# Performance work log

Measured on AMD Instinct MI355X. Metric: run time of the kernel, lower is better.

## Reference

```python
import jax, jax.numpy as jnp
import numpy as np

N = 50000
E = 800000
IN_DIM = 128
HID = 64
HEADS = 4
OUT_DIM = 128


def setup_inputs() -> dict:
    key = jax.random.key(0)
    ks = jax.random.split(key, 12)
    s = lambda fan: 1.0 / np.sqrt(fan)
    return {
        'features': jax.random.normal(ks[0], (N, IN_DIM), jnp.float32),
        'edge_index': jax.random.randint(ks[1], (2, E), 0, N, jnp.int64),
        # layer 1: in_dim -> heads*hid, concat=True
        'W1': jax.random.normal(ks[2], (IN_DIM, HEADS * HID), jnp.float32) * s(IN_DIM),
        'att_src1': jax.random.normal(ks[3], (HEADS, HID), jnp.float32) * s(HID),
        'att_dst1': jax.random.normal(ks[4], (HEADS, HID), jnp.float32) * s(HID),
        'bias1': jnp.zeros((HEADS * HID,), jnp.float32),
        # layer 2: heads*hid -> out_dim, 1 head, concat=False
        'W2': jax.random.normal(ks[5], (HEADS * HID, OUT_DIM), jnp.float32) * s(HEADS * HID),
        'att_src2': jax.random.normal(ks[6], (1, OUT_DIM), jnp.float32) * s(OUT_DIM),
        'att_dst2': jax.random.normal(ks[7], (1, OUT_DIM), jnp.float32) * s(OUT_DIM),
        'bias2': jnp.zeros((OUT_DIM,), jnp.float32),
    }


def _gat_conv(x, src, dst, W, a_src, a_dst, bias, heads, out_ch):
    n = x.shape[0]
    h = (x @ W).reshape(n, heads, out_ch)              # [N, H, C]
    alpha_s = jnp.einsum('nhc,hc->nh', h, a_src)       # [N, H]
    alpha_d = jnp.einsum('nhc,hc->nh', h, a_dst)
    e = jax.nn.leaky_relu(alpha_s[src] + alpha_d[dst], 0.2)  # [E, H]
    # segment softmax over incoming edges of each dst node
    m = jax.ops.segment_max(e, dst, num_segments=n)
    m = jnp.where(jnp.isfinite(m), m, 0.0)
    ex = jnp.exp(e - m[dst])
    denom = jax.ops.segment_sum(ex, dst, num_segments=n)
    alpha = ex / denom[dst]                            # [E, H]
    out = jax.ops.segment_sum(alpha[:, :, None] * h[src], dst, num_segments=n)  # [N, H, C]
    return out.reshape(n, heads * out_ch) + bias


def reference(features, edge_index, W1, att_src1, att_dst1, bias1, W2, att_src2, att_dst2, bias2):
    n = features.shape[0]
    loops = jnp.arange(n, dtype=edge_index.dtype)
    src = jnp.concatenate([edge_index[0], loops])
    dst = jnp.concatenate([edge_index[1], loops])

    act = lambda v: jax.nn.leaky_relu(v, 0.2)
    x = _gat_conv(features, src, dst, W1, att_src1, att_dst1, bias1, HEADS, HID)
    x = act(x)  # dropout inactive (eval)
    x = _gat_conv(x, src, dst, W2, att_src2, att_dst2, bias2, 1, OUT_DIM)
    x = act(x)
    # in_dim == out_dim -> identity residual
    return x + features
```

## Files before the change

kernel.cpp:

```cpp
#include <hip/hip_runtime.h>
#include <math.h>

#define LRELU(x) ((x) > 0.0f ? (x) : 0.2f * (x))

typedef __attribute__((ext_vector_type(8))) short bf16x8;
typedef __attribute__((ext_vector_type(4))) float floatx4;
typedef __attribute__((ext_vector_type(2))) float f32x2;

__device__ __forceinline__ float bf2f(ushort u) {
    union { unsigned u; float f; } v; v.u = ((unsigned)u) << 16; return v.f;
}
__device__ __forceinline__ ushort f2bf(float f) {
    union { float f; unsigned u; } v; v.f = f;
    unsigned r = (v.u + 0x7FFFu + ((v.u >> 16) & 1u)) >> 16;
    return (ushort)r;
}
__device__ __forceinline__ f32x2 bfpair(unsigned w) {
    union { unsigned u; float f; } lo, hi;
    lo.u = w << 16; hi.u = w & 0xffff0000u;
    return (f32x2){lo.f, hi.f};
}

__global__ __launch_bounds__(256) void prep_kernel(
    const float* __restrict__ feat, const float* __restrict__ W1,
    const float* __restrict__ as1, const float* __restrict__ ad1,
    const float* __restrict__ W2, const float* __restrict__ as2,
    const float* __restrict__ ad2, const int* __restrict__ ei,
    ushort* __restrict__ featb, ushort* __restrict__ Bp1, ushort* __restrict__ Bp2,
    int* __restrict__ deg, ushort* __restrict__ col,
    int N, int E, int Npart, int b_fil, int b_cvt, int b_p1)
{
    const int b = blockIdx.x, t = threadIdx.x;
    if (b < b_fil) {
        const int fb = b;
        const int part = fb & 7;
        const int base = (fb >> 3) * 2048;
        const int lo = part * Npart;
        const int hi = min(N, lo + Npart);
        for (int q0 = 0; q0 < 8; q0 += 4) {
            int dsts[4]; bool val[4];
#pragma unroll
            for (int u = 0; u < 4; ++u) {
                int k = base + (q0 + u) * 256 + t;
                val[u] = k < E;
                if (val[u]) dsts[u] = ei[E + k];
            }
#pragma unroll
            for (int u = 0; u < 4; ++u) {
                if (val[u] && dsts[u] >= lo && dsts[u] < hi) {
                    int k = base + (q0 + u) * 256 + t;
                    int src = ei[k];
                    int slot = atomicAdd(&deg[dsts[u]], 1);
                    if (slot < 63) col[dsts[u] * 64 + slot] = (ushort)src;
                }
            }
        }
    } else if (b < b_fil + b_cvt) {
        int i = (b - b_fil) * 256 + t;
        if (i < N * 32) {
            float4 v = ((const float4*)feat)[i];
            ushort4 o;
            o.x = f2bf(v.x); o.y = f2bf(v.y); o.z = f2bf(v.z); o.w = f2bf(v.w);
            ((ushort4*)featb)[i] = o;
        }
    } else if (b < b_fil + b_cvt + b_p1) {
        int i = (b - b_fil - b_cvt) * 256 + t;
        if (i < 272 * 128) {
            int n = i / 128, k = i % 128;
            float v;
            if (n < 256) v = W1[k * 256 + n];
            else if (n < 260) {
                int h = n - 256; float s = 0.f;
                for (int c = 0; c < 64; ++c) s += W1[k * 256 + h * 64 + c] * as1[h * 64 + c];
                v = s;
            } else if (n < 264) {
                int h = n - 260; float s = 0.f;
                for (int c = 0; c < 64; ++c) s += W1[k * 256 + h * 64 + c] * ad1[h * 64 + c];
                v = s;
            } else v = 0.f;
            Bp1[i] = f2bf(v);
        }
    } else {
        int i = (b - b_fil - b_cvt - b_p1) * 256 + t;
        if (i < 144 * 256) {
            int n = i / 256, k = i % 256;
            float v;
            if (n < 128) v = W2[k * 128 + n];
            else if (n == 128) {
                float s = 0.f;
                for (int c = 0; c < 128; ++c) s += W2[k * 128 + c] * as2[c];
                v = s;
            } else if (n == 129) {
                float s = 0.f;
                for (int c = 0; c < 128; ++c) s += W2[k * 128 + c] * ad2[c];
                v = s;
            } else v = 0.f;
            Bp2[i] = f2bf(v);
        }
    }
}

__global__ __launch_bounds__(256) void gemm_attn1_kernel(
    const ushort* __restrict__ A, const ushort* __restrict__ Bp,
    float* __restrict__ as_, float* __restrict__ ad_, int M)
{
    const int lane = threadIdx.x & 63;
    const int wave = threadIdx.x >> 6;
    const int quad = lane >> 4;
    const int l16  = lane & 15;
    const int row0 = blockIdx.x * 64 + wave * 16;
    const int arow = min(row0 + l16, M - 1);
    const ushort* ap = A + (size_t)arow * 128 + quad * 8;
    const ushort* bp = Bp + (size_t)(256 + l16) * 128 + quad * 8;

    floatx4 acc = (floatx4){0.f, 0.f, 0.f, 0.f};
#pragma unroll
    for (int k0 = 0; k0 < 128; k0 += 32) {
        bf16x8 a = *(const bf16x8*)(ap + k0);
        bf16x8 b = *(const bf16x8*)(bp + k0);
        acc = __builtin_amdgcn_mfma_f32_16x16x32_bf16(a, b, acc, 0, 0, 0);
    }
#pragma unroll
    for (int r = 0; r < 4; ++r) {
        int row = row0 + quad * 4 + r;
        if (row < M) {
            float v = acc[r];
            if (l16 < 4)      as_[row * 4 + l16] = v;
            else if (l16 < 8) ad_[row * 4 + (l16 - 4)] = v;
        }
    }
}

#define G1_LOAD(jb, u)                                                        \
    {                                                                         \
        _Pragma("unroll")                                                     \
        for (int q = 0; q < 4; ++q) {                                         \
            int jj = (jb) + 2 * q + esl;                                      \
            if (jj < dg) {                                                    \
                int s_ = __shfl(src, jj, 64);                                 \
                u[q] = *(const uint2*)(xb + (size_t)s_ * 128 + ch0);          \
            }                                                                 \
        }                                                                     \
    }
#define G1_CONSUME(jb, u)                                                     \
    {                                                                         \
        _Pragma("unroll")                                                     \
        for (int q = 0; q < 4; ++q) {                                         \
            int jj = (jb) + 2 * q + esl;                                      \
            if (jj < dg) {                                                    \
                float4 a = alph[wave][jj];                                    \
                f32x2 xlo = bfpair(u[q].x), xhi = bfpair(u[q].y);             \
                accA[0] += (f32x2){a.x, a.x} * xlo; accB[0] += (f32x2){a.x, a.x} * xhi; \
                accA[1] += (f32x2){a.y, a.y} * xlo; accB[1] += (f32x2){a.y, a.y} * xhi; \
                accA[2] += (f32x2){a.z, a.z} * xlo; accB[2] += (f32x2){a.z, a.z} * xhi; \
                accA[3] += (f32x2){a.w, a.w} * xlo; accB[3] += (f32x2){a.w, a.w} * xhi; \
            }                                                                 \
        }                                                                     \
    }

__global__ __launch_bounds__(256, 8) void gat_gather1_kernel(
    const int* __restrict__ deg, const ushort* __restrict__ col,
    const float* __restrict__ as_, const float* __restrict__ ad_,
    const ushort* __restrict__ xb, ushort* __restrict__ aggx, int N)
{
    __shared__ float4 alph[4][64];
    const int lane = threadIdx.x & 63;
    const int wave = threadIdx.x >> 6;
    const int n = blockIdx.x * 4 + wave;
    if (n >= N) return;
    const int dgE = min(deg[n], 63);
    const float4 ad4 = *(const float4*)(ad_ + n * 4);

    int src = n;
    float4 ex4 = {0.f, 0.f, 0.f, 0.f};
    if (lane <= dgE) {
        if (lane < dgE) src = col[n * 64 + lane];
        float4 a4 = *(const float4*)(as_ + src * 4);
        ex4.x = __expf(LRELU(a4.x + ad4.x));
        ex4.y = __expf(LRELU(a4.y + ad4.y));
        ex4.z = __expf(LRELU(a4.z + ad4.z));
        ex4.w = __expf(LRELU(a4.w + ad4.w));
        alph[wave][lane] = ex4;
    }
    float sx = ex4.x, sy = ex4.y, sz = ex4.z, sw = ex4.w;
#pragma unroll
    for (int m = 1; m < 64; m <<= 1) {
        sx += __shfl_xor(sx, m, 64); sy += __shfl_xor(sy, m, 64);
        sz += __shfl_xor(sz, m, 64); sw += __shfl_xor(sw, m, 64);
    }
    const float rd0 = 1.0f / sx, rd1 = 1.0f / sy, rd2 = 1.0f / sz, rd3 = 1.0f / sw;

    const int esl = lane >> 5;
    const int ch0 = (lane & 31) * 4;
    const int dg = dgE + 1;
    f32x2 accA[4] = {{0.f,0.f},{0.f,0.f},{0.f,0.f},{0.f,0.f}};
    f32x2 accB[4] = {{0.f,0.f},{0.f,0.f},{0.f,0.f},{0.f,0.f}};

    uint2 u1[4], u2[4];

    G1_LOAD(0, u1);
    for (int j0 = 0; j0 < dg; j0 += 16) {
        G1_LOAD(j0 + 8, u2);
        G1_CONSUME(j0, u1);
        G1_LOAD(j0 + 16, u1);
        G1_CONSUME(j0 + 8, u2);
    }

#pragma unroll
    for (int h = 0; h < 4; ++h) {
        accA[h].x += __shfl_xor(accA[h].x, 32, 64); accA[h].y += __shfl_xor(accA[h].y, 32, 64);
        accB[h].x += __shfl_xor(accB[h].x, 32, 64); accB[h].y += __shfl_xor(accB[h].y, 32, 64);
    }

    if (lane < 32) {
        const float rd[4] = {rd0, rd1, rd2, rd3};
#pragma unroll
        for (int h = 0; h < 4; ++h) {
            ushort4 o;
            o.x = f2bf(accA[h].x * rd[h]); o.y = f2bf(accA[h].y * rd[h]);
            o.z = f2bf(accB[h].x * rd[h]); o.w = f2bf(accB[h].y * rd[h]);
            *(ushort4*)(aggx + ((size_t)h * N + n) * 128 + ch0) = o;
        }
    }
}

__device__ __forceinline__ void l2_tile(int ct, const ushort x1s[64][264],
    const ushort* __restrict__ Bp2, int brow, int M, int lane,
    ushort* __restrict__ h2b, float* __restrict__ as2_, float* __restrict__ ad2_)
{
    const int quad = lane >> 4;
    const int l16  = lane & 15;
    bf16x8 bfr[8];
#pragma unroll
    for (int kq = 0; kq < 8; ++kq)
        bfr[kq] = *(const bf16x8*)(Bp2 + (size_t)(ct * 16 + l16) * 256 + kq * 32 + quad * 8);

    floatx4 acc[4];
#pragma unroll
    for (int rg = 0; rg < 4; ++rg) acc[rg] = (floatx4){0.f, 0.f, 0.f, 0.f};
#pragma unroll
    for (int kq = 0; kq < 8; ++kq) {
#pragma unroll
        for (int rg = 0; rg < 4; ++rg) {
            bf16x8 a = *(const bf16x8*)&x1s[rg * 16 + l16][kq * 32 + quad * 8];
            acc[rg] = __builtin_amdgcn_mfma_f32_16x16x32_bf16(a, bfr[kq], acc[rg], 0, 0, 0);
        }
    }
    if (ct < 8) {
#pragma unroll
        for (int rg = 0; rg < 4; ++rg)
#pragma unroll
            for (int r = 0; r < 4; ++r) {
                int row = brow + rg * 16 + quad * 4 + r;
                if (row < M) h2b[(size_t)row * 128 + ct * 16 + l16] = f2bf(acc[rg][r]);
            }
    } else {
#pragma unroll
        for (int rg = 0; rg < 4; ++rg)
#pragma unroll
            for (int r = 0; r < 4; ++r) {
                int row = brow + rg * 16 + quad * 4 + r;
                if (row < M) {
                    if (l16 == 0)      as2_[row] = acc[rg][r];
                    else if (l16 == 1) ad2_[row] = acc[rg][r];
                }
            }
    }
}

__global__ __launch_bounds__(256) void gemm_l1l2_kernel(
    const ushort* __restrict__ aggx, const ushort* __restrict__ Bp1,
    const float* __restrict__ bias1, const ushort* __restrict__ Bp2,
    ushort* __restrict__ h2b, float* __restrict__ as2_, float* __restrict__ ad2_, int M)
{
    __shared__ ushort x1s[64][264];
    const int lane = threadIdx.x & 63;
    const int wave = threadIdx.x >> 6;
    const int quad = lane >> 4;
    const int l16  = lane & 15;
    const int brow = blockIdx.x * 64;

    bf16x8 bfr[4][4];
#pragma unroll
    for (int nt = 0; nt < 4; ++nt)
#pragma unroll
        for (int kq = 0; kq < 4; ++kq)
            bfr[nt][kq] = *(const bf16x8*)(Bp1 + (size_t)(wave * 64 + nt * 16 + l16) * 128 + kq * 32 + quad * 8);

    bf16x8 afr[4][4];
#pragma unroll
    for (int rt = 0; rt < 4; ++rt) {
        const int arow = min(brow + rt * 16 + l16, M - 1);
        const ushort* ap = aggx + ((size_t)wave * M + arow) * 128 + quad * 8;
#pragma unroll
        for (int kq = 0; kq < 4; ++kq)
            afr[rt][kq] = *(const bf16x8*)(ap + kq * 32);
    }

#pragma unroll
    for (int rt = 0; rt < 4; ++rt) {
        floatx4 acc[4];
#pragma unroll
        for (int nt = 0; nt < 4; ++nt) acc[nt] = (floatx4){0.f, 0.f, 0.f, 0.f};
#pragma unroll
        for (int kq = 0; kq < 4; ++kq)
#pragma unroll
            for (int nt = 0; nt < 4; ++nt)
                acc[nt] = __builtin_amdgcn_mfma_f32_16x16x32_bf16(afr[rt][kq], bfr[nt][kq], acc[nt], 0, 0, 0);
#pragma unroll
        for (int nt = 0; nt < 4; ++nt) {
            const int c = wave * 64 + nt * 16 + l16;
            const float bv = bias1[c];
#pragma unroll
            for (int r = 0; r < 4; ++r)
                x1s[rt * 16 + quad * 4 + r][c] = f2bf(LRELU(acc[nt][r] + bv));
        }
    }
    __syncthreads();

    l2_tile(wave * 2,     x1s, Bp2, brow, M, lane, h2b, as2_, ad2_);
    l2_tile(wave * 2 + 1, x1s, Bp2, brow, M, lane, h2b, as2_, ad2_);
    if (wave == 3)
        l2_tile(8,        x1s, Bp2, brow, M, lane, h2b, as2_, ad2_);
}

#define G2_LOAD(jb, u)                                                        \
    {                                                                         \
        _Pragma("unroll")                                                     \
        for (int q = 0; q < 4; ++q) {                                         \
            int jj = (jb) + 2 * q + esl;                                      \
            if (jj < dg) {                                                    \
                int s_ = __shfl(src, jj, 64);                                 \
                u[q] = *(const uint2*)(h2 + (size_t)s_ * 128 + ch0);          \
            }                                                                 \
        }                                                                     \
    }
#define G2_CONSUME(jb, u)                                                     \
    {                                                                         \
        _Pragma("unroll")                                                     \
        for (int q = 0; q < 4; ++q) {                                         \
            int jj = (jb) + 2 * q + esl;                                      \
            if (jj < dg) {                                                    \
                float a = alph[wave][jj];                                     \
                accA += (f32x2){a, a} * bfpair(u[q].x);                       \
                accB += (f32x2){a, a} * bfpair(u[q].y);                       \
            }                                                                 \
        }                                                                     \
    }

__global__ __launch_bounds__(256, 8) void gat_gather2_kernel(
    const int* __restrict__ deg, const ushort* __restrict__ col,
    const float* __restrict__ as_, const float* __restrict__ ad_,
    const ushort* __restrict__ h2, const float* __restrict__ bias,
    const float* __restrict__ resid, float* __restrict__ out, int N)
{
    __shared__ float alph[4][64];
    const int lane = threadIdx.x & 63;
    const int wave = threadIdx.x >> 6;
    const int n = blockIdx.x * 4 + wave;
    if (n >= N) return;
    const int dgE = min(deg[n], 63);
    const float adv = ad_[n];

    int src = n;
    float ex = 0.f;
    if (lane <= dgE) {
        if (lane < dgE) src = col[n * 64 + lane];
        ex = __expf(LRELU(as_[src] + adv));
        alph[wave][lane] = ex;
    }
    float s = ex;
#pragma unroll
    for (int m = 1; m < 64; m <<= 1) s += __shfl_xor(s, m, 64);
    const float rden = 1.0f / s;

    const int esl = lane >> 5;
    const int ch0 = (lane & 31) * 4;
    const int dg = dgE + 1;
    f32x2 accA = {0.f, 0.f}, accB = {0.f, 0.f};

    uint2 u1[4], u2[4];

    G2_LOAD(0, u1);
    for (int j0 = 0; j0 < dg; j0 += 16) {
        G2_LOAD(j0 + 8, u2);
        G2_CONSUME(j0, u1);
        G2_LOAD(j0 + 16, u1);
        G2_CONSUME(j0 + 8, u2);
    }

    accA.x += __shfl_xor(accA.x, 32, 64); accA.y += __shfl_xor(accA.y, 32, 64);
    accB.x += __shfl_xor(accB.x, 32, 64); accB.y += __shfl_xor(accB.y, 32, 64);

    if (lane < 32) {
        const float4 bv = *(const float4*)(bias + ch0);
        const float4 fv = *(const float4*)(resid + (size_t)n * 128 + ch0);
        float4 o;
        o.x = LRELU(accA.x * rden + bv.x) + fv.x;
        o.y = LRELU(accA.y * rden + bv.y) + fv.y;
        o.z = LRELU(accB.x * rden + bv.z) + fv.z;
        o.w = LRELU(accB.y * rden + bv.w) + fv.w;
        *(float4*)(out + (size_t)n * 128 + ch0) = o;
    }
}

extern "C" void kernel_launch(void* const* d_in, const int* in_sizes, int n_in,
                              void* d_out, int out_size, void* d_ws, size_t ws_size,
                              hipStream_t stream)
{
    const float* feat = (const float*)d_in[0];
    const int*   ei   = (const int*)d_in[1];
    const float* W1   = (const float*)d_in[2];
    const float* asrc1 = (const float*)d_in[3];
    const float* adst1 = (const float*)d_in[4];
    const float* bias1 = (const float*)d_in[5];
    const float* W2    = (const float*)d_in[6];
    const float* asrc2 = (const float*)d_in[7];
    const float* adst2 = (const float*)d_in[8];
    const float* bias2 = (const float*)d_in[9];
    float* outp = (float*)d_out;

    const int IN_DIM = 128, C2 = 128;
    const int N = in_sizes[0] / IN_DIM;
    const int E = in_sizes[1] / 2;

    char* w = (char*)d_ws;
    ushort* featb = (ushort*)w; w += (size_t)N * IN_DIM * 2;
    ushort* aggx  = (ushort*)w; w += (size_t)4 * N * IN_DIM * 2;
    ushort* h2b   = (ushort*)w; w += (size_t)N * C2 * 2;
    ushort* Bp1   = (ushort*)w; w += (size_t)272 * 128 * 2;
    ushort* Bp2   = (ushort*)w; w += (size_t)144 * 256 * 2;
    float* as1_   = (float*)w;  w += (size_t)N * 4 * 4;
    float* ad1_   = (float*)w;  w += (size_t)N * 4 * 4;
    float* as2_   = (float*)w;  w += (size_t)N * 4;
    float* ad2_   = (float*)w;  w += (size_t)N * 4;
    int* deg      = (int*)w;    w += (size_t)N * 4;
    ushort* col   = (ushort*)w; w += (size_t)N * 64 * 2;

    dim3 blk(256);
    const int mg = (N + 63) / 64;
    const int gg = (N + 3) / 4;
    const int Npart = (N + 7) / 8;

    const int b_cvt = (N * 32 + 255) / 256;
    const int b_p1  = (272 * 128 + 255) / 256;
    const int b_p2  = (144 * 256 + 255) / 256;
    const int b_fil = 8 * ((E + 2047) / 2048);

    hipMemsetAsync(deg, 0, (size_t)N * 4, stream);
    prep_kernel<<<dim3(b_fil + b_cvt + b_p1 + b_p2), blk, 0, stream>>>(
        feat, W1, asrc1, adst1, W2, asrc2, adst2, ei,
        featb, Bp1, Bp2, deg, col, N, E, Npart, b_fil, b_cvt, b_p1);

    gemm_attn1_kernel<<<dim3(mg), blk, 0, stream>>>(featb, Bp1, as1_, ad1_, N);
    gat_gather1_kernel<<<dim3(gg), blk, 0, stream>>>(deg, col, as1_, ad1_, featb, aggx, N);

    gemm_l1l2_kernel<<<dim3(mg), blk, 0, stream>>>(aggx, Bp1, bias1, Bp2, h2b, as2_, ad2_, N);

    gat_gather2_kernel<<<dim3(gg), blk, 0, stream>>>(deg, col, as2_, ad2_, h2b, bias2, feat, outp, N);
}
```

Baseline: 261.8 us.

## Branchless padded gather loops with inline-asm loads; halve edges per fill block

```diff
diff --git a/kernel.cpp b/kernel.cpp
--- a/kernel.cpp
+++ b/kernel.cpp
@@ -7,9 +7,6 @@
 typedef __attribute__((ext_vector_type(4))) float floatx4;
 typedef __attribute__((ext_vector_type(2))) float f32x2;
 
-__device__ __forceinline__ float bf2f(ushort u) {
-    union { unsigned u; float f; } v; v.u = ((unsigned)u) << 16; return v.f;
-}
 __device__ __forceinline__ ushort f2bf(float f) {
     union { float f; unsigned u; } v; v.f = f;
     unsigned r = (v.u + 0x7FFFu + ((v.u >> 16) & 1u)) >> 16;
@@ -34,25 +31,23 @@
     if (b < b_fil) {
         const int fb = b;
         const int part = fb & 7;
-        const int base = (fb >> 3) * 2048;
+        const int base = (fb >> 3) * 1024;
         const int lo = part * Npart;
         const int hi = min(N, lo + Npart);
-        for (int q0 = 0; q0 < 8; q0 += 4) {
-            int dsts[4]; bool val[4];
-#pragma unroll
-            for (int u = 0; u < 4; ++u) {
-                int k = base + (q0 + u) * 256 + t;
-                val[u] = k < E;
-                if (val[u]) dsts[u] = ei[E + k];
-            }
-#pragma unroll
-            for (int u = 0; u < 4; ++u) {
-                if (val[u] && dsts[u] >= lo && dsts[u] < hi) {
-                    int k = base + (q0 + u) * 256 + t;
-                    int src = ei[k];
-                    int slot = atomicAdd(&deg[dsts[u]], 1);
-                    if (slot < 63) col[dsts[u] * 64 + slot] = (ushort)src;
-                }
+        int dsts[4]; bool val[4];
+#pragma unroll
+        for (int u = 0; u < 4; ++u) {
+            int k = base + u * 256 + t;
+            val[u] = k < E;
+            if (val[u]) dsts[u] = ei[E + k];
+        }
+#pragma unroll
+        for (int u = 0; u < 4; ++u) {
+            if (val[u] && dsts[u] >= lo && dsts[u] < hi) {
+                int k = base + u * 256 + t;
+                int src = ei[k];
+                int slot = atomicAdd(&deg[dsts[u]], 1);
+                if (slot < 63) col[dsts[u] * 64 + slot] = (ushort)src;
             }
         }
     } else if (b < b_fil + b_cvt) {
@@ -131,34 +126,7 @@
     }
 }
 
-#define G1_LOAD(jb, u)                                                        \
-    {                                                                         \
-        _Pragma("unroll")                                                     \
-        for (int q = 0; q < 4; ++q) {                                         \
-            int jj = (jb) + 2 * q + esl;                                      \
-            if (jj < dg) {                                                    \
-                int s_ = __shfl(src, jj, 64);                                 \
-                u[q] = *(const uint2*)(xb + (size_t)s_ * 128 + ch0);          \
-            }                                                                 \
-        }                                                                     \
-    }
-#define G1_CONSUME(jb, u)                                                     \
-    {                                                                         \
-        _Pragma("unroll")                                                     \
-        for (int q = 0; q < 4; ++q) {                                         \
-            int jj = (jb) + 2 * q + esl;                                      \
-            if (jj < dg) {                                                    \
-                float4 a = alph[wave][jj];                                    \
-                f32x2 xlo = bfpair(u[q].x), xhi = bfpair(u[q].y);             \
-                accA[0] += (f32x2){a.x, a.x} * xlo; accB[0] += (f32x2){a.x, a.x} * xhi; \
-                accA[1] += (f32x2){a.y, a.y} * xlo; accB[1] += (f32x2){a.y, a.y} * xhi; \
-                accA[2] += (f32x2){a.z, a.z} * xlo; accB[2] += (f32x2){a.z, a.z} * xhi; \
-                accA[3] += (f32x2){a.w, a.w} * xlo; accB[3] += (f32x2){a.w, a.w} * xhi; \
-            }                                                                 \
-        }                                                                     \
-    }
-
-__global__ __launch_bounds__(256, 8) void gat_gather1_kernel(
+__global__ __launch_bounds__(256) void gat_gather1_kernel(
     const int* __restrict__ deg, const ushort* __restrict__ col,
     const float* __restrict__ as_, const float* __restrict__ ad_,
     const ushort* __restrict__ xb, ushort* __restrict__ aggx, int N)
@@ -180,8 +148,8 @@
         ex4.y = __expf(LRELU(a4.y + ad4.y));
         ex4.z = __expf(LRELU(a4.z + ad4.z));
         ex4.w = __expf(LRELU(a4.w + ad4.w));
-        alph[wave][lane] = ex4;
-    }
+    }
+    alph[wave][lane] = ex4;
     float sx = ex4.x, sy = ex4.y, sz = ex4.z, sw = ex4.w;
 #pragma unroll
     for (int m = 1; m < 64; m <<= 1) {
@@ -193,17 +161,44 @@
     const int esl = lane >> 5;
     const int ch0 = (lane & 31) * 4;
     const int dg = dgE + 1;
+    const int dgR = (dg + 15) & ~15;
     f32x2 accA[4] = {{0.f,0.f},{0.f,0.f},{0.f,0.f},{0.f,0.f}};
     f32x2 accB[4] = {{0.f,0.f},{0.f,0.f},{0.f,0.f},{0.f,0.f}};
 
     uint2 u1[4], u2[4];
 
-    G1_LOAD(0, u1);
-    for (int j0 = 0; j0 < dg; j0 += 16) {
-        G1_LOAD(j0 + 8, u2);
-        G1_CONSUME(j0, u1);
-        G1_LOAD(j0 + 16, u1);
-        G1_CONSUME(j0 + 8, u2);
+#define G1_LOAD4(jb, u)                                                       \
+    {                                                                         \
+        _Pragma("unroll")                                                     \
+        for (int q = 0; q < 4; ++q) {                                         \
+            int jj = (jb) + 2 * q + esl;               \
+            int s_ = __shfl(src, jj, 64);                                     \
+            const ushort* p_ = xb + (size_t)s_ * 128 + ch0;                   \
+            asm volatile("global_load_dwordx2 %0, %1, off"                    \
+                         : "=v"(u[q]) : "v"(p_));                             \
+        }                                                                     \
+    }
+#define G1_CONS4(jb, u)                                                       \
+    {                                                                         \
+        _Pragma("unroll")                                                     \
+        for (int q = 0; q < 4; ++q) {                                         \
+            int jj = (jb) + 2 * q + esl;                                      \
+            float4 a = alph[wave][jj];                                        \
+            f32x2 xlo = bfpair(u[q].x), xhi = bfpair(u[q].y);                 \
+            accA[0] += (f32x2){a.x, a.x} * xlo; accB[0] += (f32x2){a.x, a.x} * xhi; \
+            accA[1] += (f32x2){a.y, a.y} * xlo; accB[1] += (f32x2){a.y, a.y} * xhi; \
+            accA[2] += (f32x2){a.z, a.z} * xlo; accB[2] += (f32x2){a.z, a.z} * xhi; \
+            accA[3] += (f32x2){a.w, a.w} * xlo; accB[3] += (f32x2){a.w, a.w} * xhi; \
+        }                                                                     \
+    }
+
+    for (int j0 = 0; j0 < dgR; j0 += 16) {
+        G1_LOAD4(j0, u1);
+        G1_LOAD4(j0 + 8, u2);
+        asm volatile("s_waitcnt vmcnt(0)" ::: "memory");
+        __builtin_amdgcn_sched_barrier(0);
+        G1_CONS4(j0, u1);
+        G1_CONS4(j0 + 8, u2);
     }
 
 #pragma unroll
@@ -324,31 +319,7 @@
         l2_tile(8,        x1s, Bp2, brow, M, lane, h2b, as2_, ad2_);
 }
 
-#define G2_LOAD(jb, u)                                                        \
-    {                                                                         \
-        _Pragma("unroll")                                                     \
-        for (int q = 0; q < 4; ++q) {                                         \
-            int jj = (jb) + 2 * q + esl;                                      \
-            if (jj < dg) {                                                    \
-                int s_ = __shfl(src, jj, 64);                                 \
-                u[q] = *(const uint2*)(h2 + (size_t)s_ * 128 + ch0);          \
-            }                                                                 \
-        }                                                                     \
-    }
-#define G2_CONSUME(jb, u)                                                     \
-    {                                                                         \
-        _Pragma("unroll")                                                     \
-        for (int q = 0; q < 4; ++q) {                                         \
-            int jj = (jb) + 2 * q + esl;                                      \
-            if (jj < dg) {                                                    \
-                float a = alph[wave][jj];                                     \
-                accA += (f32x2){a, a} * bfpair(u[q].x);                       \
-                accB += (f32x2){a, a} * bfpair(u[q].y);                       \
-            }                                                                 \
-        }                                                                     \
-    }
-
-__global__ __launch_bounds__(256, 8) void gat_gather2_kernel(
+__global__ __launch_bounds__(256) void gat_gather2_kernel(
     const int* __restrict__ deg, const ushort* __restrict__ col,
     const float* __restrict__ as_, const float* __restrict__ ad_,
     const ushort* __restrict__ h2, const float* __restrict__ bias,
@@ -367,8 +338,8 @@
     if (lane <= dgE) {
         if (lane < dgE) src = col[n * 64 + lane];
         ex = __expf(LRELU(as_[src] + adv));
-        alph[wave][lane] = ex;
-    }
+    }
+    alph[wave][lane] = ex;
     float s = ex;
 #pragma unroll
     for (int m = 1; m < 64; m <<= 1) s += __shfl_xor(s, m, 64);
@@ -377,16 +348,40 @@
     const int esl = lane >> 5;
     const int ch0 = (lane & 31) * 4;
     const int dg = dgE + 1;
+    const int dgR = (dg + 15) & ~15;
     f32x2 accA = {0.f, 0.f}, accB = {0.f, 0.f};
 
     uint2 u1[4], u2[4];
 
-    G2_LOAD(0, u1);
-    for (int j0 = 0; j0 < dg; j0 += 16) {
-        G2_LOAD(j0 + 8, u2);
-        G2_CONSUME(j0, u1);
-        G2_LOAD(j0 + 16, u1);
-        G2_CONSUME(j0 + 8, u2);
+#define G2_LOAD4(jb, u)                                                       \
+    {                                                                         \
+        _Pragma("unroll")                                                     \
+        for (int q = 0; q < 4; ++q) {                                         \
+            int jj = (jb) + 2 * q + esl;                                      \
+            int s_ = __shfl(src, jj, 64);                                     \
+            const ushort* p_ = h2 + (size_t)s_ * 128 + ch0;                   \
+            asm volatile("global_load_dwordx2 %0, %1, off"                    \
+                         : "=v"(u[q]) : "v"(p_));                             \
+        }                                                                     \
+    }
+#define G2_CONS4(jb, u)                                                       \
+    {                                                                         \
+        _Pragma("unroll")                                                     \
+        for (int q = 0; q < 4; ++q) {                                         \
+            int jj = (jb) + 2 * q + esl;                                      \
+            float a = alph[wave][jj];                                         \
+            accA += (f32x2){a, a} * bfpair(u[q].x);                           \
+            accB += (f32x2){a, a} * bfpair(u[q].y);                           \
+        }                                                                     \
+    }
+
+    for (int j0 = 0; j0 < dgR; j0 += 16) {
+        G2_LOAD4(j0, u1);
+        G2_LOAD4(j0 + 8, u2);
+        asm volatile("s_waitcnt vmcnt(0)" ::: "memory");
+        __builtin_amdgcn_sched_barrier(0);
+        G2_CONS4(j0, u1);
+        G2_CONS4(j0 + 8, u2);
     }
 
     accA.x += __shfl_xor(accA.x, 32, 64); accA.y += __shfl_xor(accA.y, 32, 64);
@@ -445,7 +440,7 @@
     const int b_cvt = (N * 32 + 255) / 256;
     const int b_p1  = (272 * 128 + 255) / 256;
     const int b_p2  = (144 * 256 + 255) / 256;
-    const int b_fil = 8 * ((E + 2047) / 2048);
+    const int b_fil = 8 * ((E + 1023) / 1024);
 
     hipMemsetAsync(deg, 0, (size_t)N * 4, stream);
     prep_kernel<<<dim3(b_fil + b_cvt + b_p1 + b_p2), blk, 0, stream>>>(
```

New measurement: 251.1 us. 4.1% less time.
